# Kernel tuning notes

Measured on AMD Instinct MI355X. Metric: run time of the kernel, lower is better.

## Reference

```python
import jax, jax.numpy as jnp
import numpy as np

C = 1.0  # Poincare ball curvature


def _artanh(x):
    return jnp.arctanh(jnp.clip(x, -1 + 1e-5, 1 - 1e-5))


def _expmap0(u, c=C):
    sc = jnp.sqrt(jnp.float32(c))
    n = jnp.clip(jnp.linalg.norm(u, axis=-1, keepdims=True), 1e-15)
    return jnp.tanh(sc * n) * u / (sc * n)


def _logmap0(x, c=C):
    sc = jnp.sqrt(jnp.float32(c))
    n = jnp.clip(jnp.linalg.norm(x, axis=-1, keepdims=True), 1e-15)
    return _artanh(sc * n) * x / (sc * n)


def _mobius_add(x, y, c=C):
    x2 = jnp.sum(x * x, -1, keepdims=True)
    y2 = jnp.sum(y * y, -1, keepdims=True)
    xy = jnp.sum(x * y, -1, keepdims=True)
    num = (1 + 2 * c * xy + c * y2) * x + (1 - c * x2) * y
    den = 1 + 2 * c * xy + c * c * x2 * y2
    return num / jnp.clip(den, 1e-15)


def _mobius_matvec(M, x, c=C):
    sc = jnp.sqrt(jnp.float32(c))
    xn = jnp.clip(jnp.linalg.norm(x, axis=-1, keepdims=True), 1e-15)
    Mx = x @ M.T
    Mxn = jnp.clip(jnp.linalg.norm(Mx, axis=-1, keepdims=True), 1e-15)
    return jnp.tanh(Mxn / xn * _artanh(sc * xn)) * Mx / (sc * Mxn)


def _dist2_all(x, y, c=C):
    # x: [N, D] points on ball, y: [K, D] codebook points -> [N, K] squared dists
    # dist(x,y) = 2/sqrt(c) * artanh(sqrt(c) * ||(-x) (+) y||)
    # ||(-x) (+) y|| computed from dot products only (no [N,K,D] intermediate):
    #   (-x) (+) y = (a*(-x) + b*y) / den,
    #   a = 1 - 2c<x,y> + c|y|^2,  b = 1 - c|x|^2,  den = 1 - 2c<x,y> + c^2|x|^2|y|^2
    x2 = jnp.sum(x * x, -1)[:, None]           # [N,1]
    y2 = jnp.sum(y * y, -1)[None, :]           # [1,K]
    xy = x @ y.T                               # [N,K] (the big matmul)
    a = 1 - 2 * c * xy + c * y2
    b = 1 - c * x2
    den = 1 - 2 * c * xy + c * c * x2 * y2
    num2 = a * a * x2 - 2 * a * b * xy + b * b * y2
    norm = jnp.sqrt(jnp.clip(num2, 0.0)) / jnp.clip(den, 1e-15)
    d = (2.0 / jnp.sqrt(jnp.float32(c))) * _artanh(jnp.sqrt(jnp.float32(c)) * norm)
    return d * d


def setup_inputs() -> dict:
    key = jax.random.key(0)
    k0, k1, k2, k3, k4 = jax.random.split(key, 5)
    B, S, D, K = 16, 128, 128, 32000
    v_tangent = 0.1 * jax.random.normal(k0, (B, S, D), jnp.float32)
    code_points = _expmap0(0.1 * jax.random.normal(k1, (K, D), jnp.float32))
    W = jax.random.normal(k2, (D, D), jnp.float32) / jnp.sqrt(jnp.float32(D))
    b = 0.01 * jax.random.normal(k3, (D,), jnp.float32)
    freq = jax.random.uniform(k4, (K,), jnp.float32) * 1000.0
    fb = jnp.log(freq + 1.0)
    freq_bias = (fb - fb.mean()) * 0.5
    return {"v_tangent": v_tangent, "code_points": code_points, "W": W,
            "b": b, "freq_bias": freq_bias, "temperature": jnp.float32(1.0)}


def reference(v_tangent, code_points, W, b, freq_bias, temperature):
    batch_shape = v_tangent.shape[:-1]
    D = v_tangent.shape[-1]
    v = v_tangent.reshape(-1, D)
    # tiny hyperbolic linear layer (1-layer Poincare MLP = Mobius matvec + Mobius bias add)
    p = _expmap0(v)
    p = _mobius_add(_mobius_matvec(W, p), _expmap0(b[None, :]))
    v = _logmap0(p)
    # back onto the manifold, distance-based logits vs full codebook
    p = _expmap0(v)
    logits = -_dist2_all(p, code_points) / (temperature * temperature)
    logits = logits + freq_bias[None, :]
    return logits.reshape(*batch_shape, -1)
```

## Files before the change

### kernel.cpp

```cpp
#include <hip/hip_runtime.h>
#include <hip/hip_bf16.h>


typedef __attribute__((ext_vector_type(8))) short short8;
typedef __attribute__((ext_vector_type(4))) float f32x4;
typedef unsigned short u16;

__device__ inline float bits2f(unsigned u){ union{unsigned u; float f;} x; x.u=u; return x.f; }
__device__ inline u16 f2bf(float f){
  union { float f; unsigned u; } x; x.f = f;
  unsigned r = x.u + 0x7fff + ((x.u >> 16) & 1);
  return (u16)(r >> 16);
}
__device__ inline void bfsplit(float f, u16 &h, u16 &l){
  u16 hb = f2bf(f);
  float hf = bits2f(((unsigned)hb) << 16);
  h = hb;
  l = f2bf(f - hf);
}

__device__ inline float wred(float x){
#pragma unroll
  for (int off = 32; off; off >>= 1) x += __shfl_xor(x, off, 64);
  return x;
}
__device__ inline float wred32(float x){
#pragma unroll
  for (int off = 16; off; off >>= 1) x += __shfl_xor(x, off, 64);
  return x;
}

__device__ inline float dotW(const float* __restrict__ w, const float* __restrict__ p){
  float m = 0.f;
#pragma unroll
  for (int i = 0; i < 32; ++i){
    float4 u = *(const float4*)(w + 4*i);
    const float* q = p + 4*i;
    m = fmaf(u.x, q[0], m); m = fmaf(u.y, q[1], m);
    m = fmaf(u.z, q[2], m); m = fmaf(u.w, q[3], m);
  }
  return m;
}

__global__ __launch_bounds__(64) void prep_kernel(
    const float* __restrict__ vt, const float* __restrict__ Wm,
    const float* __restrict__ bias,
    u16* __restrict__ ahi, u16* __restrict__ alo, float* __restrict__ x2o)
{
  const int row = blockIdx.x, lane = threadIdx.x;
  const int e0 = 2*lane;
  const float CLIP = 0.99999f;

  float v0 = vt[row*128 + e0];
  float v1 = vt[row*128 + e0 + 1];
  float n1 = fmaxf(sqrtf(wred(v0*v0 + v1*v1)), 1e-15f);
  float s1 = tanhf(n1)/n1;
  float p0 = s1*v0, p1 = s1*v1;
  __shared__ float sP[128];
  sP[e0] = p0; sP[e0+1] = p1;
  __syncthreads();
  float xn = fmaxf(sqrtf(wred(p0*p0 + p1*p1)), 1e-15f);
  float mx0 = dotW(Wm + e0*128, sP);
  float mx1 = dotW(Wm + (e0+1)*128, sP);
  float Mxn = fmaxf(sqrtf(wred(mx0*mx0 + mx1*mx1)), 1e-15f);
  float smv = tanhf((Mxn/xn) * atanhf(fminf(xn, CLIP))) / Mxn;
  float m0 = smv*mx0, m1 = smv*mx1;
  float b0 = bias[e0], b1 = bias[e0+1];
  float nb = fmaxf(sqrtf(wred(b0*b0 + b1*b1)), 1e-15f);
  float sb = tanhf(nb)/nb;
  float eb0 = sb*b0, eb1 = sb*b1;
  float x2m = wred(m0*m0 + m1*m1);
  float y2e = wred(eb0*eb0 + eb1*eb1);
  float xy  = wred(m0*eb0 + m1*eb1);
  float ca = 1.f + 2.f*xy + y2e;
  float cb = 1.f - x2m;
  float den = fmaxf(1.f + 2.f*xy + x2m*y2e, 1e-15f);
  float q0 = (ca*m0 + cb*eb0)/den, q1 = (ca*m1 + cb*eb1)/den;
  float n2 = fmaxf(sqrtf(wred(q0*q0 + q1*q1)), 1e-15f);
  float u = atanhf(fminf(n2, CLIP));
  float sv = u/n2;
  float w0v = sv*q0, w1v = sv*q1;
  float n3 = fmaxf(sqrtf(wred(w0v*w0v + w1v*w1v)), 1e-15f);
  float s3 = tanhf(n3)/n3;
  float P0 = s3*w0v, P1 = s3*w1v;
  float x2v = wred(P0*P0 + P1*P1);
  u16 h0, l0, h1, l1;
  bfsplit(P0, h0, l0); bfsplit(P1, h1, l1);
  ahi[row*128 + e0] = h0; ahi[row*128 + e0 + 1] = h1;
  alo[row*128 + e0] = l0; alo[row*128 + e0 + 1] = l1;
  if (lane == 0) x2o[row] = x2v;
}

__global__ __launch_bounds__(256) void split_y2_kernel(
    const float* __restrict__ code, u16* __restrict__ Bh,
    u16* __restrict__ Bl, float* __restrict__ y2o)
{
  const int c = threadIdx.x & 31, r = threadIdx.x >> 5;
  const int row = blockIdx.x*8 + r;
  float4 u = *(const float4*)(code + (size_t)row*128 + c*4);
  u16 h0,h1,h2,h3,l0,l1,l2,l3;
  bfsplit(u.x,h0,l0); bfsplit(u.y,h1,l1);
  bfsplit(u.z,h2,l2); bfsplit(u.w,h3,l3);
  ushort4 hv; hv.x=h0; hv.y=h1; hv.z=h2; hv.w=h3;
  ushort4 lv; lv.x=l0; lv.y=l1; lv.z=l2; lv.w=l3;
  *(ushort4*)(Bh + (size_t)row*128 + c*4) = hv;
  *(ushort4*)(Bl + (size_t)row*128 + c*4) = lv;
  float s = fmaf(u.x,u.x, fmaf(u.y,u.y, fmaf(u.z,u.z, u.w*u.w)));
  s = wred32(s);
  if (c == 0) y2o[row] = s;
}

#define SBS 136

__global__ __launch_bounds__(256, 3) void decode_main(
    const u16* __restrict__ Bh_g, const u16* __restrict__ Bl_g,
    const u16* __restrict__ ahi_g, const u16* __restrict__ alo_g,
    const float* __restrict__ x2g, const float* __restrict__ y2g,
    const float* __restrict__ fbg, const float* __restrict__ tempg,
    float* __restrict__ outp)
{
  __shared__ u16 sBh[64*SBS];
  __shared__ u16 sBl[64*SBS];
  const int tid  = threadIdx.x;
  const int wave = tid >> 6, lane = tid & 63;
  const int quad = lane >> 4, l16 = lane & 15;
  const int m0 = blockIdx.x*64 + wave*16;
  const int arow = m0 + l16;

  short8 ah[4], al[4];
#pragma unroll
  for (int ks = 0; ks < 4; ++ks){
    ah[ks] = *(const short8*)(ahi_g + arow*128 + ks*32 + quad*8);
    al[ks] = *(const short8*)(alo_g + arow*128 + ks*32 + quad*8);
  }
  const float xv  = x2g[arow];
  const float bb  = 1.f - xv;
  const float ntb = -2.f*bb;
  const float b2  = bb*bb;
  const float tmp  = tempg[0];
  const float nit2 = -1.f/(tmp*tmp);
  const int n_base = blockIdx.y*256;

  for (int rnd = 0; rnd < 4; ++rnd){
    const int n0r = n_base + rnd*64;
    __syncthreads();
#pragma unroll
    for (int i = 0; i < 4; ++i){
      int id = tid + i*256;
      int c = id >> 4, sg = id & 15;
      size_t goff = (size_t)(n0r + c)*128 + sg*8;
      *(uint4*)(&sBh[c*SBS + sg*8]) = *(const uint4*)(Bh_g + goff);
      *(uint4*)(&sBl[c*SBS + sg*8]) = *(const uint4*)(Bl_g + goff);
    }
    __syncthreads();
#pragma unroll
    for (int ct = 0; ct < 4; ++ct){
      const int ccol = ct*16 + l16;
      short8 bh[4], bl[4];
#pragma unroll
      for (int ks = 0; ks < 4; ++ks){
        bh[ks] = *(const short8*)(&sBh[ccol*SBS + ks*32 + quad*8]);
        bl[ks] = *(const short8*)(&sBl[ccol*SBS + ks*32 + quad*8]);
      }
      f32x4 acch = {0.f,0.f,0.f,0.f}, accx = {0.f,0.f,0.f,0.f};
#pragma unroll
      for (int ks = 0; ks < 4; ++ks){
        acch = __builtin_amdgcn_mfma_f32_16x16x32_bf16(bh[ks], ah[ks], acch, 0, 0, 0);
        accx = __builtin_amdgcn_mfma_f32_16x16x32_bf16(bl[ks], ah[ks], accx, 0, 0, 0);
        accx = __builtin_amdgcn_mfma_f32_16x16x32_bf16(bh[ks], al[ks], accx, 0, 0, 0);
      }
      const int cbase = n0r + ct*16 + quad*4;
      const float4 y2v4 = *(const float4*)(y2g + cbase);
      const float4 fbv4 = *(const float4*)(fbg + cbase);
      float4 o;
#pragma unroll
      for (int r = 0; r < 4; ++r){
        float y2v = ((const float*)&y2v4)[r];
        float t   = acch[r] + accx[r];
        float two = t + t;
        float a   = (1.f + y2v) - two;
        float den = fmaf(xv, y2v, 1.f - two);
        float dc  = fmaxf(den, 1e-15f);
        float num2 = fmaf(a*xv, a, fmaf(ntb*t, a, b2*y2v));
        float sq  = sqrtf(fmaxf(num2, 0.f));
        float s   = fminf(sq, 0.99999f*dc);
        float d   = __logf(__fdividef(dc + s, dc - s));
        ((float*)&o)[r] = fmaf(d*d, nit2, ((const float*)&fbv4)[r]);
      }
      *(float4*)(outp + (size_t)arow*32000 + cbase) = o;
    }
  }
}

extern "C" void kernel_launch(void* const* d_in, const int* in_sizes, int n_in,
                              void* d_out, int out_size, void* d_ws, size_t ws_size,
                              hipStream_t stream) {
  const float* vt   = (const float*)d_in[0];
  const float* code = (const float*)d_in[1];
  const float* Wm   = (const float*)d_in[2];
  const float* bias = (const float*)d_in[3];
  const float* fb   = (const float*)d_in[4];
  const float* temp = (const float*)d_in[5];
  float* outp = (float*)d_out;

  char* ws = (char*)d_ws;
  u16*   ahi = (u16*)ws;
  u16*   alo = (u16*)(ws + 512*1024);
  float* x2  = (float*)(ws + 1024*1024);
  float* y2  = (float*)(ws + 1024*1024 + 8192);
  u16*   Bh  = (u16*)(ws + 1280*1024);
  u16*   Bl  = (u16*)(ws + 1280*1024 + 8192*1024);

  prep_kernel<<<2048, 64, 0, stream>>>(vt, Wm, bias, ahi, alo, x2);
  split_y2_kernel<<<4000, 256, 0, stream>>>(code, Bh, Bl, y2);
  dim3 grid(32, 125);
  decode_main<<<grid, 256, 0, stream>>>(Bh, Bl, ahi, alo, x2, y2, fb, temp, outp);
}
```

Baseline: 444.9 us.

## Switch decode GEMM to 32x32 MFMA tiles with direct global-to-LDS swizzled loads

The main decode kernel now uses 32x32x16 bf16 MFMA instructions, with each block covering 128 rows instead of 64, so the grid is halved. The codebook tile is loaded straight into LDS with global_load_lds and an XOR swizzle replaces the padded layout. The log is switched to log2 with the ln2^2 factor folded into the temperature scale. This aims to cut LDS traffic and load instructions per output and to improve reuse of the B tile. In exchange each thread holds more accumulator registers, and the output store pattern changes.

```diff
diff --git a/kernel.cpp b/kernel.cpp
--- a/kernel.cpp
+++ b/kernel.cpp
@@ -3,8 +3,9 @@
 
 
 typedef __attribute__((ext_vector_type(8))) short short8;
-typedef __attribute__((ext_vector_type(4))) float f32x4;
+typedef __attribute__((ext_vector_type(16))) float f32x16;
 typedef unsigned short u16;
+typedef unsigned int u32;
 
 __device__ inline float bits2f(unsigned u){ union{unsigned u; float f;} x; x.u=u; return x.f; }
 __device__ inline u16 f2bf(float f){
@@ -40,6 +41,12 @@
     m = fmaf(u.z, q[2], m); m = fmaf(u.w, q[3], m);
   }
   return m;
+}
+
+__device__ inline void gl_lds16(const u16* g, u16* l){
+  __builtin_amdgcn_global_load_lds(
+      (const __attribute__((address_space(1))) u32*)g,
+      (__attribute__((address_space(3))) u32*)l, 16, 0, 0);
 }
 
 __global__ __launch_bounds__(64) void prep_kernel(
@@ -110,8 +117,6 @@
   if (c == 0) y2o[row] = s;
 }
 
-#define SBS 136
-
 __global__ __launch_bounds__(256, 3) void decode_main(
     const u16* __restrict__ Bh_g, const u16* __restrict__ Bl_g,
     const u16* __restrict__ ahi_g, const u16* __restrict__ alo_g,
@@ -119,75 +124,92 @@
     const float* __restrict__ fbg, const float* __restrict__ tempg,
     float* __restrict__ outp)
 {
-  __shared__ u16 sBh[64*SBS];
-  __shared__ u16 sBl[64*SBS];
+  __shared__ __align__(16) u16 sBh[64*128];
+  __shared__ __align__(16) u16 sBl[64*128];
   const int tid  = threadIdx.x;
   const int wave = tid >> 6, lane = tid & 63;
-  const int quad = lane >> 4, l16 = lane & 15;
-  const int m0 = blockIdx.x*64 + wave*16;
-  const int arow = m0 + l16;
-
-  short8 ah[4], al[4];
-#pragma unroll
-  for (int ks = 0; ks < 4; ++ks){
-    ah[ks] = *(const short8*)(ahi_g + arow*128 + ks*32 + quad*8);
-    al[ks] = *(const short8*)(alo_g + arow*128 + ks*32 + quad*8);
+  const int l32  = lane & 31, half = lane >> 5;
+  const int m0   = blockIdx.x*128 + wave*32;
+  const int arow = m0 + l32;
+
+  short8 ah[8], al[8];
+#pragma unroll
+  for (int ks = 0; ks < 8; ++ks){
+    ah[ks] = *(const short8*)(ahi_g + (size_t)arow*128 + ks*16 + half*8);
+    al[ks] = *(const short8*)(alo_g + (size_t)arow*128 + ks*16 + half*8);
   }
   const float xv  = x2g[arow];
   const float bb  = 1.f - xv;
   const float ntb = -2.f*bb;
   const float b2  = bb*bb;
-  const float tmp  = tempg[0];
-  const float nit2 = -1.f/(tmp*tmp);
+  const float tmp = tempg[0];
+  const float nit2 = -0.4804530139182014f/(tmp*tmp);
   const int n_base = blockIdx.y*256;
+
+  int s_col[4], s_swz[4], s_ldb[4];
+#pragma unroll
+  for (int it = 0; it < 4; ++it){
+    int id = it*256 + tid;
+    s_col[it] = id >> 4;
+    int sg = id & 15;
+    s_swz[it] = ((sg*16) ^ ((s_col[it] & 7) << 4)) >> 1;
+    s_ldb[it] = (it*256 + (tid & ~63)) * 8;
+  }
 
   for (int rnd = 0; rnd < 4; ++rnd){
     const int n0r = n_base + rnd*64;
     __syncthreads();
 #pragma unroll
-    for (int i = 0; i < 4; ++i){
-      int id = tid + i*256;
-      int c = id >> 4, sg = id & 15;
-      size_t goff = (size_t)(n0r + c)*128 + sg*8;
-      *(uint4*)(&sBh[c*SBS + sg*8]) = *(const uint4*)(Bh_g + goff);
-      *(uint4*)(&sBl[c*SBS + sg*8]) = *(const uint4*)(Bl_g + goff);
+    for (int it = 0; it < 4; ++it){
+      size_t gb = (size_t)(n0r + s_col[it])*128 + s_swz[it];
+      gl_lds16(Bh_g + gb, &sBh[s_ldb[it]]);
+    }
+#pragma unroll
+    for (int it = 0; it < 4; ++it){
+      size_t gb = (size_t)(n0r + s_col[it])*128 + s_swz[it];
+      gl_lds16(Bl_g + gb, &sBl[s_ldb[it]]);
     }
     __syncthreads();
-#pragma unroll
-    for (int ct = 0; ct < 4; ++ct){
-      const int ccol = ct*16 + l16;
-      short8 bh[4], bl[4];
-#pragma unroll
-      for (int ks = 0; ks < 4; ++ks){
-        bh[ks] = *(const short8*)(&sBh[ccol*SBS + ks*32 + quad*8]);
-        bl[ks] = *(const short8*)(&sBl[ccol*SBS + ks*32 + quad*8]);
+
+#pragma unroll
+    for (int ct = 0; ct < 2; ++ct){
+      const int ccol = ct*32 + l32;
+      f32x16 acch = {0.f,0.f,0.f,0.f,0.f,0.f,0.f,0.f,0.f,0.f,0.f,0.f,0.f,0.f,0.f,0.f};
+      f32x16 accx = {0.f,0.f,0.f,0.f,0.f,0.f,0.f,0.f,0.f,0.f,0.f,0.f,0.f,0.f,0.f,0.f};
+#pragma unroll
+      for (int ks = 0; ks < 8; ++ks){
+        int kb  = ks*32 + half*16;
+        int off = (ccol*256 + (kb ^ ((ccol & 7) << 4))) >> 1;
+        short8 bh = *(const short8*)(&sBh[off]);
+        short8 bl = *(const short8*)(&sBl[off]);
+        acch = __builtin_amdgcn_mfma_f32_32x32x16_bf16(bh, ah[ks], acch, 0, 0, 0);
+        accx = __builtin_amdgcn_mfma_f32_32x32x16_bf16(bl, ah[ks], accx, 0, 0, 0);
+        accx = __builtin_amdgcn_mfma_f32_32x32x16_bf16(bh, al[ks], accx, 0, 0, 0);
       }
-      f32x4 acch = {0.f,0.f,0.f,0.f}, accx = {0.f,0.f,0.f,0.f};
-#pragma unroll
-      for (int ks = 0; ks < 4; ++ks){
-        acch = __builtin_amdgcn_mfma_f32_16x16x32_bf16(bh[ks], ah[ks], acch, 0, 0, 0);
-        accx = __builtin_amdgcn_mfma_f32_16x16x32_bf16(bl[ks], ah[ks], accx, 0, 0, 0);
-        accx = __builtin_amdgcn_mfma_f32_16x16x32_bf16(bh[ks], al[ks], accx, 0, 0, 0);
+      const int cb = n0r + ct*32 + half*4;
+#pragma unroll
+      for (int g = 0; g < 4; ++g){
+        const int cg = cb + g*8;
+        const float4 y2v4 = *(const float4*)(y2g + cg);
+        const float4 fbv4 = *(const float4*)(fbg + cg);
+        float4 o;
+#pragma unroll
+        for (int q = 0; q < 4; ++q){
+          const int r = g*4 + q;
+          float y2v = ((const float*)&y2v4)[q];
+          float t   = acch[r] + accx[r];
+          float two = t + t;
+          float a   = (1.f + y2v) - two;
+          float den = fmaf(xv, y2v, 1.f - two);
+          float dc  = fmaxf(den, 1e-15f);
+          float num2 = fmaf(a*xv, a, fmaf(ntb*t, a, b2*y2v));
+          float sq  = sqrtf(fmaxf(num2, 0.f));
+          float s   = fminf(sq, 0.99999f*dc);
+          float lg  = __log2f(__fdividef(dc + s, dc - s));
+          ((float*)&o)[q] = fmaf(lg*lg, nit2, ((const float*)&fbv4)[q]);
+        }
+        *(float4*)(outp + (size_t)arow*32000 + cg) = o;
       }
-      const int cbase = n0r + ct*16 + quad*4;
-      const float4 y2v4 = *(const float4*)(y2g + cbase);
-      const float4 fbv4 = *(const float4*)(fbg + cbase);
-      float4 o;
-#pragma unroll
-      for (int r = 0; r < 4; ++r){
-        float y2v = ((const float*)&y2v4)[r];
-        float t   = acch[r] + accx[r];
-        float two = t + t;
-        float a   = (1.f + y2v) - two;
-        float den = fmaf(xv, y2v, 1.f - two);
-        float dc  = fmaxf(den, 1e-15f);
-        float num2 = fmaf(a*xv, a, fmaf(ntb*t, a, b2*y2v));
-        float sq  = sqrtf(fmaxf(num2, 0.f));
-        float s   = fminf(sq, 0.99999f*dc);
-        float d   = __logf(__fdividef(dc + s, dc - s));
-        ((float*)&o)[r] = fmaf(d*d, nit2, ((const float*)&fbv4)[r]);
-      }
-      *(float4*)(outp + (size_t)arow*32000 + cbase) = o;
     }
   }
 }
@@ -213,6 +235,6 @@
 
   prep_kernel<<<2048, 64, 0, stream>>>(vt, Wm, bias, ahi, alo, x2);
   split_y2_kernel<<<4000, 256, 0, stream>>>(code, Bh, Bl, y2);
-  dim3 grid(32, 125);
+  dim3 grid(16, 125);
   decode_main<<<grid, 256, 0, stream>>>(Bh, Bl, ahi, alo, x2, y2, fb, temp, outp);
 }
```

Result: no change. 445.6 us (+0.2%).
